# Performance work log

Measured on AMD Instinct MI355X. Metric: run time of the kernel, lower is better.

## Reference

```python
import jax, jax.numpy as jnp
import numpy as np

N = 100000
F_IN = 128
H = 64
E = 3200000


def setup_inputs() -> dict:
    key = jax.random.key(0)
    ks = jax.random.split(key, 10)
    x = jax.random.normal(ks[0], (N, F_IN), dtype=jnp.float32)
    edge_index = jax.random.randint(ks[1], (2, E), 0, N, dtype=jnp.int64)
    hidden_state = jax.random.normal(ks[2], (1, N, H), dtype=jnp.float32)
    # GCNConv params (glorot-ish scale)
    W_gcn = jax.random.normal(ks[3], (F_IN, H), dtype=jnp.float32) / np.sqrt(F_IN)
    b_gcn = jnp.zeros((H,), dtype=jnp.float32)
    # torch.nn.GRU params, layout [3H, in] with gate order (r, z, n)
    s = 1.0 / np.sqrt(H)
    W_ih = jax.random.uniform(ks[4], (3 * H, H), dtype=jnp.float32, minval=-s, maxval=s)
    W_hh = jax.random.uniform(ks[5], (3 * H, H), dtype=jnp.float32, minval=-s, maxval=s)
    b_ih = jax.random.uniform(ks[6], (3 * H,), dtype=jnp.float32, minval=-s, maxval=s)
    b_hh = jax.random.uniform(ks[7], (3 * H,), dtype=jnp.float32, minval=-s, maxval=s)
    return {"x": x, "edge_index": edge_index, "hidden_state": hidden_state,
            "W_gcn": W_gcn, "b_gcn": b_gcn,
            "W_ih": W_ih, "W_hh": W_hh, "b_ih": b_ih, "b_hh": b_hh}


def gcn_conv(x, edge_index, W, b):
    n = x.shape[0]
    # add self-loops (PyG GCNConv default)
    loops = jnp.arange(n, dtype=edge_index.dtype)
    row = jnp.concatenate([edge_index[0], loops])  # source
    col = jnp.concatenate([edge_index[1], loops])  # target
    # symmetric normalization: deg over targets with unit edge weights
    deg = jax.ops.segment_sum(jnp.ones_like(col, dtype=x.dtype), col, num_segments=n)
    dis = jnp.where(deg > 0, jax.lax.rsqrt(deg), 0.0)
    norm = dis[row] * dis[col]  # (E+N,)
    xt = x @ W  # (N, H) transform first, then aggregate
    msg = norm[:, None] * xt[row]  # (E+N, H)
    out = jax.ops.segment_sum(msg, col, num_segments=n)
    return out + b


def gru_step(x, h, W_ih, W_hh, b_ih, b_hh):
    # single-step torch GRU, gate order (r, z, n)
    gi = x @ W_ih.T + b_ih  # (N, 3H)
    gh = h @ W_hh.T + b_hh
    i_r, i_z, i_n = jnp.split(gi, 3, axis=-1)
    h_r, h_z, h_n = jnp.split(gh, 3, axis=-1)
    r = jax.nn.sigmoid(i_r + h_r)
    z = jax.nn.sigmoid(i_z + h_z)
    n = jnp.tanh(i_n + r * h_n)
    return (1.0 - z) * n + z * h


def reference(x, edge_index, hidden_state, W_gcn, b_gcn, W_ih, W_hh, b_ih, b_hh):
    g = jax.nn.relu(gcn_conv(x, edge_index, W_gcn, b_gcn))  # (N, H)
    h_new = gru_step(g, hidden_state[0], W_ih, W_hh, b_ih, b_hh)  # (N, H)
    return h_new, h_new[None]  # (out, new_hidden_state)
```

## Files before the change

### kernel.cpp

```cpp
#include <hip/hip_runtime.h>
#include <cmath>

constexpr int NN  = 100000;
constexpr int FIN = 128;
constexpr int HH  = 64;
constexpr int NE  = 3200000;
constexpr int NB  = (NN + 255) / 256;
constexpr int NFB  = NB;
constexpr int PCAP = 10240;

typedef __attribute__((ext_vector_type(8))) short short8;
typedef __attribute__((ext_vector_type(4))) float f32x4;

__device__ __forceinline__ ushort f2bf(float x) {
    unsigned u = __float_as_uint(x);
    u += 0x7FFF + ((u >> 16) & 1);
    return (ushort)(u >> 16);
}
__device__ __forceinline__ float bf2f(ushort h) {
    return __uint_as_float(((unsigned)h) << 16);
}
__device__ __forceinline__ unsigned pack2(float a, float b) {
    return (unsigned)f2bf(a) | ((unsigned)f2bf(b) << 16);
}

__global__ void __launch_bounds__(256) k_part(const int* __restrict__ ei,
                                              int* __restrict__ gcnt,
                                              int* __restrict__ pairs) {
    __shared__ int lcnt[NFB];
    __shared__ int lbase[NFB];
    int t = threadIdx.x;
    for (int i = t; i < NFB; i += 256) lcnt[i] = 0;
    __syncthreads();

    long long base = (long long)blockIdx.x * 8192;
    int4 r4[8], c4[8];
    int nv[8];
#pragma unroll
    for (int s = 0; s < 8; ++s) {
        long long e = base + s * 1024 + t * 4;
        if (e < NE) {
            r4[s] = ((const int4*)(ei))[e >> 2];
            c4[s] = ((const int4*)(ei + NE))[e >> 2];
            nv[s] = 1;
            atomicAdd(&lcnt[c4[s].x >> 8], 1);
            atomicAdd(&lcnt[c4[s].y >> 8], 1);
            atomicAdd(&lcnt[c4[s].z >> 8], 1);
            atomicAdd(&lcnt[c4[s].w >> 8], 1);
        } else {
            nv[s] = 0;
        }
    }
    __syncthreads();
    for (int i = t; i < NFB; i += 256) {
        int c = lcnt[i];
        lbase[i] = c ? atomicAdd(&gcnt[i], c) : 0;
        lcnt[i] = 0;
    }
    __syncthreads();
#pragma unroll
    for (int s = 0; s < 8; ++s) {
        if (!nv[s]) continue;
        int rr[4] = {r4[s].x, r4[s].y, r4[s].z, r4[s].w};
        int cc[4] = {c4[s].x, c4[s].y, c4[s].z, c4[s].w};
#pragma unroll
        for (int k = 0; k < 4; ++k) {
            int b   = cc[k] >> 8;
            int p   = atomicAdd(&lcnt[b], 1);
            int pos = lbase[b] + p;
            if (pos < PCAP) pairs[b * PCAP + pos] = (rr[k] << 8) | (cc[k] & 255);
        }
    }
}

__global__ void __launch_bounds__(256) k_csr(const int* __restrict__ pairs,
                                             const int* __restrict__ gcnt,
                                             int* __restrict__ deg,
                                             int* __restrict__ rowptr,
                                             float* __restrict__ dis,
                                             int* __restrict__ csr) {
    __shared__ int sg[256];
    __shared__ int ldeg[256];
    __shared__ int lrp[256];
    __shared__ int lcur[256];
    __shared__ int lcsr[PCAP];
    int f = blockIdx.x;
    int t = threadIdx.x;
    int partial = 0;
    if (t < f) partial += gcnt[t];
    if (t + 256 < f) partial += gcnt[t + 256];
    sg[t] = partial;
    ldeg[t] = 0;
    __syncthreads();
    for (int off = 128; off > 0; off >>= 1) {
        if (t < off) sg[t] += sg[t + off];
        __syncthreads();
    }
    int base = sg[0];
    int cnt  = min(gcnt[f], PCAP);
    int n0   = f * 256;
    const int* pb = pairs + f * PCAP;
    for (int i = t; i < cnt; i += 256) atomicAdd(&ldeg[pb[i] & 255], 1);
    __syncthreads();
    int v = ldeg[t];
    lrp[t] = v;
    __syncthreads();
    for (int off = 1; off < 256; off <<= 1) {
        int add = (t >= off) ? lrp[t - off] : 0;
        __syncthreads();
        lrp[t] += add;
        __syncthreads();
    }
    int excl = lrp[t] - v;
    if (n0 + t < NN) {
        deg[n0 + t]    = v;
        rowptr[n0 + t] = base + excl;
        dis[n0 + t]    = rsqrtf((float)(v + 1));
    }
    lcur[t] = excl;
    __syncthreads();
    for (int i = t; i < cnt; i += 256) {
        int e = pb[i];
        int p = atomicAdd(&lcur[e & 255], 1);
        lcsr[p] = e >> 8;
    }
    __syncthreads();
    for (int i = t; i < cnt; i += 256) csr[base + i] = lcsr[i];
}

__global__ void __launch_bounds__(256) k_xt(const float* __restrict__ x,
                                            const ushort* __restrict__ wgx,
                                            const float* __restrict__ dis,
                                            ushort* __restrict__ xtb) {
    __shared__ ushort Ahi[64 * 136];
    __shared__ ushort Alo[64 * 136];
    __shared__ float sdis[64];
    const ushort* GXhi = wgx;
    const ushort* GXlo = wgx + 64 * 128;
    int t  = threadIdx.x;
    int r0 = blockIdx.x * 64;
    if (t < 64) sdis[t] = (r0 + t < NN) ? dis[r0 + t] : 0.f;
    unsigned* Ahi32 = (unsigned*)Ahi;
    unsigned* Alo32 = (unsigned*)Alo;
#pragma unroll
    for (int s = 0; s < 8; ++s) {
        int idx = t + 256 * s;
        int nd  = idx >> 5;
        int kq  = idx & 31;
        bool ok = (r0 + nd) < NN;
        float4 v = ok ? ((const float4*)(x + (size_t)(r0 + nd) * FIN))[kq]
                      : make_float4(0.f, 0.f, 0.f, 0.f);
        int b2 = nd * 68 + kq * 2;
        float hx = bf2f(f2bf(v.x)), hy = bf2f(f2bf(v.y));
        float hz = bf2f(f2bf(v.z)), hw = bf2f(f2bf(v.w));
        Ahi32[b2]     = pack2(v.x, v.y);
        Ahi32[b2 + 1] = pack2(v.z, v.w);
        Alo32[b2]     = pack2(v.x - hx, v.y - hy);
        Alo32[b2 + 1] = pack2(v.z - hz, v.w - hw);
    }
    __syncthreads();

    int lane = t & 63, w = t >> 6, l15 = lane & 15;
    int kbase = (lane >> 4) * 8;
    int j = w * 16 + l15;
    f32x4 acc[4];
#pragma unroll
    for (int m = 0; m < 4; ++m) acc[m] = (f32x4){0.f, 0.f, 0.f, 0.f};
    short8 bh[4], bl[4];
#pragma unroll
    for (int ks = 0; ks < 4; ++ks) {
        bh[ks] = *(const short8*)(GXhi + j * 128 + ks * 32 + kbase);
        bl[ks] = *(const short8*)(GXlo + j * 128 + ks * 32 + kbase);
    }
#pragma unroll
    for (int mt = 0; mt < 4; ++mt) {
        int abase = (mt * 16 + l15) * 136 + kbase;
#pragma unroll
        for (int ks = 0; ks < 4; ++ks) {
            short8 ah = *(const short8*)&Ahi[abase + ks * 32];
            short8 al = *(const short8*)&Alo[abase + ks * 32];
            acc[mt] = __builtin_amdgcn_mfma_f32_16x16x32_bf16(ah, bh[ks], acc[mt], 0, 0, 0);
            acc[mt] = __builtin_amdgcn_mfma_f32_16x16x32_bf16(al, bh[ks], acc[mt], 0, 0, 0);
            acc[mt] = __builtin_amdgcn_mfma_f32_16x16x32_bf16(ah, bl[ks], acc[mt], 0, 0, 0);
        }
    }
    __syncthreads();
#pragma unroll
    for (int mt = 0; mt < 4; ++mt) {
#pragma unroll
        for (int reg = 0; reg < 4; ++reg) {
            int row = mt * 16 + (lane >> 4) * 4 + reg;
            Alo[row * 64 + j] = f2bf(sdis[row] * acc[mt][reg]);
        }
    }
    __syncthreads();
    const uint4* src = (const uint4*)Alo;
    uint4* dst = (uint4*)(xtb + (size_t)r0 * HH);
#pragma unroll
    for (int s = 0; s < 2; ++s) {
        int u   = t + 256 * s;
        int row = u >> 3;
        if (r0 + row < NN) dst[u] = src[u];
    }
}

__global__ void __launch_bounds__(256) k_gather(const int* __restrict__ csr,
                                                const int* __restrict__ rowptr,
                                                const int* __restrict__ deg,
                                                const float* __restrict__ dis,
                                                const ushort* __restrict__ xtb,
                                                const float* __restrict__ bg,
                                                float* __restrict__ g) {
    __shared__ int lid[4][64];
    int t    = threadIdx.x;
    int lane = t & 63;
    int w    = t >> 6;
    int n    = blockIdx.x * 4 + w;
    int r = lane >> 3;
    int q = lane & 7;
    float acc[8] = {0.f, 0.f, 0.f, 0.f, 0.f, 0.f, 0.f, 0.f};
    float dn  = dis[n];
    int start = rowptr[n];
    int cnt   = deg[n];
    for (int c0 = 0; c0 < cnt; c0 += 64) {
        int m = min(64, cnt - c0);
        if (lane < m) lid[w][lane] = csr[start + c0 + lane];
        int i = r;
        for (; i + 8 < m; i += 16) {
            int s0 = lid[w][i];
            int s1 = lid[w][i + 8];
            short8 v0 = ((const short8*)(xtb + (size_t)s0 * HH))[q];
            short8 v1 = ((const short8*)(xtb + (size_t)s1 * HH))[q];
#pragma unroll
            for (int j = 0; j < 8; ++j) acc[j] += bf2f((ushort)v0[j]);
#pragma unroll
            for (int j = 0; j < 8; ++j) acc[j] += bf2f((ushort)v1[j]);
        }
        if (i < m) {
            int s0 = lid[w][i];
            short8 v0 = ((const short8*)(xtb + (size_t)s0 * HH))[q];
#pragma unroll
            for (int j = 0; j < 8; ++j) acc[j] += bf2f((ushort)v0[j]);
        }
    }
#pragma unroll
    for (int j = 0; j < 8; ++j) {
        acc[j] += __shfl_xor(acc[j], 8, 64);
        acc[j] += __shfl_xor(acc[j], 16, 64);
        acc[j] += __shfl_xor(acc[j], 32, 64);
    }
    if (r == 0) {
        short8 xs = ((const short8*)(xtb + (size_t)n * HH))[q];
        float4 b0 = ((const float4*)bg)[q * 2];
        float4 b1 = ((const float4*)bg)[q * 2 + 1];
        float bb[8] = {b0.x, b0.y, b0.z, b0.w, b1.x, b1.y, b1.z, b1.w};
        float res[8];
#pragma unroll
        for (int j = 0; j < 8; ++j)
            res[j] = fmaxf(fmaf(dn, acc[j] + bf2f((ushort)xs[j]), bb[j]), 0.f);
        float4* go = (float4*)(g + (size_t)n * HH + q * 8);
        go[0] = make_float4(res[0], res[1], res[2], res[3]);
        go[1] = make_float4(res[4], res[5], res[6], res[7]);
    }
}

__global__ void k_wprep(const float* __restrict__ Wih, const float* __restrict__ Whh,
                        const float* __restrict__ Wg, ushort* __restrict__ bsp) {
    ushort* Bhi  = bsp;
    ushort* Blo  = bsp + 192 * 128;
    ushort* BShi = bsp + 2 * 192 * 128;
    ushort* BSlo = BShi + 64 * 64;
    ushort* GXhi = BSlo + 64 * 64;
    ushort* GXlo = GXhi + 64 * 128;
    int i = blockIdx.x * 256 + threadIdx.x;
    if (i < 192 * 128) {
        int j = i >> 7, k = i & 127;
        float wv = (k < 64) ? Wih[j * 64 + k] : Whh[j * 64 + (k - 64)];
        ushort hi = f2bf(wv);
        Bhi[i] = hi;
        Blo[i] = f2bf(wv - bf2f(hi));
    }
    if (i < 64 * 64) {
        int j = i >> 6, k = i & 63;
        float wv = Whh[(128 + j) * 64 + k];
        ushort hi = f2bf(wv);
        BShi[i] = hi;
        BSlo[i] = f2bf(wv - bf2f(hi));
    }
    if (i < 64 * 128) {
        int j = i >> 7, k = i & 127;
        float wv = Wg[k * HH + j];
        ushort hi = f2bf(wv);
        GXhi[i] = hi;
        GXlo[i] = f2bf(wv - bf2f(hi));
    }
}

__global__ void __launch_bounds__(256) k_gru(
    const float* __restrict__ gbuf, const float* __restrict__ hprev,
    const ushort* __restrict__ bsp,
    const float* __restrict__ bih, const float* __restrict__ bhh,
    float* __restrict__ out) {
    __shared__ ushort Ahi[32 * 136];
    __shared__ ushort Alo[32 * 136];
    const ushort* Bhi  = bsp;
    const ushort* Blo  = bsp + 192 * 128;
    const ushort* BShi = bsp + 2 * 192 * 128;
    const ushort* BSlo = BShi + 64 * 64;

    int t  = threadIdx.x;
    int n0 = blockIdx.x * 32;

    unsigned* Ahi32 = (unsigned*)Ahi;
    unsigned* Alo32 = (unsigned*)Alo;
#pragma unroll
    for (int s = 0; s < 2; ++s) {
        int idx = t + 256 * s;
        int nd  = idx >> 4;
        int kq  = idx & 15;
        bool ok = (n0 + nd) < NN;
        float4 vg = ok ? ((const float4*)(gbuf  + (size_t)(n0 + nd) * HH))[kq]
                       : make_float4(0.f, 0.f, 0.f, 0.f);
        float4 vh = ok ? ((const float4*)(hprev + (size_t)(n0 + nd) * HH))[kq]
                       : make_float4(0.f, 0.f, 0.f, 0.f);
        int bg2 = nd * 68 + kq * 2;
        int bh2 = bg2 + 32;
        float ghx = bf2f(f2bf(vg.x)), ghy = bf2f(f2bf(vg.y));
        float ghz = bf2f(f2bf(vg.z)), ghw = bf2f(f2bf(vg.w));
        float hhx = bf2f(f2bf(vh.x)), hhy = bf2f(f2bf(vh.y));
        float hhz = bf2f(f2bf(vh.z)), hhw = bf2f(f2bf(vh.w));
        Ahi32[bg2]     = pack2(vg.x, vg.y);
        Ahi32[bg2 + 1] = pack2(vg.z, vg.w);
        Alo32[bg2]     = pack2(vg.x - ghx, vg.y - ghy);
        Alo32[bg2 + 1] = pack2(vg.z - ghz, vg.w - ghw);
        Ahi32[bh2]     = pack2(vh.x, vh.y);
        Ahi32[bh2 + 1] = pack2(vh.z, vh.w);
        Alo32[bh2]     = pack2(vh.x - hhx, vh.y - hhy);
        Alo32[bh2 + 1] = pack2(vh.z - hhz, vh.w - hhw);
    }
    __syncthreads();

    int lane  = t & 63;
    int w     = t >> 6;
    int l15   = lane & 15;
    int kbase = (lane >> 4) * 8;

    f32x4 acc[4][2];
#pragma unroll
    for (int a = 0; a < 4; ++a)
#pragma unroll
        for (int m = 0; m < 2; ++m) acc[a][m] = (f32x4){0.f, 0.f, 0.f, 0.f};

#pragma unroll
    for (int g = 0; g < 3; ++g) {
        int brow = (w + 4 * g) * 16 + l15;
        short8 bh[4], bl[4];
#pragma unroll
        for (int ks = 0; ks < 4; ++ks) {
            bh[ks] = *(const short8*)(Bhi + brow * 128 + ks * 32 + kbase);
            bl[ks] = *(const short8*)(Blo + brow * 128 + ks * 32 + kbase);
        }
#pragma unroll
        for (int mt = 0; mt < 2; ++mt) {
            int abase = (mt * 16 + l15) * 136 + kbase;
#pragma unroll
            for (int ks = 0; ks < 4; ++ks) {
                short8 ah = *(const short8*)&Ahi[abase + ks * 32];
                short8 al = *(const short8*)&Alo[abase + ks * 32];
                acc[g][mt] = __builtin_amdgcn_mfma_f32_16x16x32_bf16(ah, bh[ks], acc[g][mt], 0, 0, 0);
                acc[g][mt] = __builtin_amdgcn_mfma_f32_16x16x32_bf16(al, bh[ks], acc[g][mt], 0, 0, 0);
                acc[g][mt] = __builtin_amdgcn_mfma_f32_16x16x32_bf16(ah, bl[ks], acc[g][mt], 0, 0, 0);
            }
        }
    }
    {
        int brow = w * 16 + l15;
        short8 bh[2], bl[2];
#pragma unroll
        for (int ks = 0; ks < 2; ++ks) {
            bh[ks] = *(const short8*)(BShi + brow * 64 + ks * 32 + kbase);
            bl[ks] = *(const short8*)(BSlo + brow * 64 + ks * 32 + kbase);
        }
#pragma unroll
        for (int mt = 0; mt < 2; ++mt) {
            int abase = (mt * 16 + l15) * 136 + 64 + kbase;
#pragma unroll
            for (int ks = 0; ks < 2; ++ks) {
                short8 ah = *(const short8*)&Ahi[abase + ks * 32];
                short8 al = *(const short8*)&Alo[abase + ks * 32];
                acc[3][mt] = __builtin_amdgcn_mfma_f32_16x16x32_bf16(ah, bh[ks], acc[3][mt], 0, 0, 0);
                acc[3][mt] = __builtin_amdgcn_mfma_f32_16x16x32_bf16(al, bh[ks], acc[3][mt], 0, 0, 0);
                acc[3][mt] = __builtin_amdgcn_mfma_f32_16x16x32_bf16(ah, bl[ks], acc[3][mt], 0, 0, 0);
            }
        }
    }

    int j = 16 * w + l15;
    float br  = bih[j] + bhh[j];
    float bz  = bih[HH + j] + bhh[HH + j];
    float bin = bih[2 * HH + j];
    float bhn = bhh[2 * HH + j];
#pragma unroll
    for (int mt = 0; mt < 2; ++mt) {
#pragma unroll
        for (int reg = 0; reg < 4; ++reg) {
            int row  = mt * 16 + (lane >> 4) * 4 + reg;
            int node = n0 + row;
            if (node < NN) {
                float S1 = acc[0][mt][reg];
                float S2 = acc[1][mt][reg];
                float S3 = acc[2][mt][reg];
                float Hn = acc[3][mt][reg];
                float r  = __builtin_amdgcn_rcpf(1.f + __expf(-(S1 + br)));
                float z  = __builtin_amdgcn_rcpf(1.f + __expf(-(S2 + bz)));
                float na = (S3 - Hn + bin) + r * (Hn + bhn);
                float e2 = __expf(2.f * na);
                float nv = fmaf(-2.f, __builtin_amdgcn_rcpf(1.f + e2), 1.f);
                int lidx = row * 136 + 64 + j;
                float h  = bf2f(Ahi[lidx]) + bf2f(Alo[lidx]);
                float o  = (1.f - z) * nv + z * h;
                out[(size_t)node * HH + j] = o;
                out[(size_t)NN * HH + (size_t)node * HH + j] = o;
            }
        }
    }
}

extern "C" void kernel_launch(void* const* d_in, const int* in_sizes, int n_in,
                              void* d_out, int out_size, void* d_ws, size_t ws_size,
                              hipStream_t stream) {
    const float* x   = (const float*)d_in[0];
    const int*   ei  = (const int*)d_in[1];
    const float* hs  = (const float*)d_in[2];
    const float* Wg  = (const float*)d_in[3];
    const float* bg  = (const float*)d_in[4];
    const float* Wih = (const float*)d_in[5];
    const float* Whh = (const float*)d_in[6];
    const float* bih = (const float*)d_in[7];
    const float* bhh = (const float*)d_in[8];
    float* out = (float*)d_out;

    char* ws = (char*)d_ws;
    int*    pairs  = (int*)   (ws);
    ushort* xtb    = (ushort*)(ws);
    float*  gbuf   = (float*) (ws + 16400000);
    int*    csr    = (int*)   (ws + 42000000);
    int*    deg    = (int*)   (ws + 54800000);
    int*    rowptr = (int*)   (ws + 55200000);
    float*  dis    = (float*) (ws + 55600000);
    ushort* wsplit = (ushort*)(ws + 56000000);
    int*    gcnt   = (int*)   (ws + 56200000);

    hipMemsetAsync(gcnt, 0, NFB * sizeof(int), stream);

    hipLaunchKernelGGL(k_wprep, dim3(96), dim3(256), 0, stream, Wih, Whh, Wg, wsplit);
    hipLaunchKernelGGL(k_part,  dim3((NE + 8191) / 8192), dim3(256), 0, stream, ei, gcnt, pairs);
    hipLaunchKernelGGL(k_csr,   dim3(NFB), dim3(256), 0, stream,
                       pairs, gcnt, deg, rowptr, dis, csr);
    hipLaunchKernelGGL(k_xt,    dim3((NN + 63) / 64), dim3(256), 0, stream,
                       x, wsplit + 2 * 192 * 128 + 2 * 64 * 64, dis, xtb);
    hipLaunchKernelGGL(k_gather, dim3(NN / 4), dim3(256), 0, stream,
                       csr, rowptr, deg, dis, xtb, bg, gbuf);
    hipLaunchKernelGGL(k_gru,   dim3((NN + 31) / 32), dim3(256), 0, stream,
                       gbuf, hs, wsplit, bih, bhh, out);
}
```

Baseline: 321.3 us.

## Fuse GCN neighbor gather into GRU kernel via shared-memory staging

Merges the gather/aggregate kernel and the GRU MFMA kernel into one 512-thread kernel that handles 64 nodes per block. Each wave aggregates 8 nodes and writes the ReLU output, split into bf16 hi/lo parts, straight into shared memory, so the fp32 intermediate buffer no longer goes through global memory and one launch is removed. In exchange, each wave now walks 8 nodes serially and the block is larger with more shared memory, which may lower occupancy and reduce latency hiding for the irregular gather.

```diff
diff --git a/kernel.cpp b/kernel.cpp
--- a/kernel.cpp
+++ b/kernel.cpp
@@ -204,66 +204,6 @@
     }
 }
 
-__global__ void __launch_bounds__(256) k_gather(const int* __restrict__ csr,
-                                                const int* __restrict__ rowptr,
-                                                const int* __restrict__ deg,
-                                                const float* __restrict__ dis,
-                                                const ushort* __restrict__ xtb,
-                                                const float* __restrict__ bg,
-                                                float* __restrict__ g) {
-    __shared__ int lid[4][64];
-    int t    = threadIdx.x;
-    int lane = t & 63;
-    int w    = t >> 6;
-    int n    = blockIdx.x * 4 + w;
-    int r = lane >> 3;
-    int q = lane & 7;
-    float acc[8] = {0.f, 0.f, 0.f, 0.f, 0.f, 0.f, 0.f, 0.f};
-    float dn  = dis[n];
-    int start = rowptr[n];
-    int cnt   = deg[n];
-    for (int c0 = 0; c0 < cnt; c0 += 64) {
-        int m = min(64, cnt - c0);
-        if (lane < m) lid[w][lane] = csr[start + c0 + lane];
-        int i = r;
-        for (; i + 8 < m; i += 16) {
-            int s0 = lid[w][i];
-            int s1 = lid[w][i + 8];
-            short8 v0 = ((const short8*)(xtb + (size_t)s0 * HH))[q];
-            short8 v1 = ((const short8*)(xtb + (size_t)s1 * HH))[q];
-#pragma unroll
-            for (int j = 0; j < 8; ++j) acc[j] += bf2f((ushort)v0[j]);
-#pragma unroll
-            for (int j = 0; j < 8; ++j) acc[j] += bf2f((ushort)v1[j]);
-        }
-        if (i < m) {
-            int s0 = lid[w][i];
-            short8 v0 = ((const short8*)(xtb + (size_t)s0 * HH))[q];
-#pragma unroll
-            for (int j = 0; j < 8; ++j) acc[j] += bf2f((ushort)v0[j]);
-        }
-    }
-#pragma unroll
-    for (int j = 0; j < 8; ++j) {
-        acc[j] += __shfl_xor(acc[j], 8, 64);
-        acc[j] += __shfl_xor(acc[j], 16, 64);
-        acc[j] += __shfl_xor(acc[j], 32, 64);
-    }
-    if (r == 0) {
-        short8 xs = ((const short8*)(xtb + (size_t)n * HH))[q];
-        float4 b0 = ((const float4*)bg)[q * 2];
-        float4 b1 = ((const float4*)bg)[q * 2 + 1];
-        float bb[8] = {b0.x, b0.y, b0.z, b0.w, b1.x, b1.y, b1.z, b1.w};
-        float res[8];
-#pragma unroll
-        for (int j = 0; j < 8; ++j)
-            res[j] = fmaxf(fmaf(dn, acc[j] + bf2f((ushort)xs[j]), bb[j]), 0.f);
-        float4* go = (float4*)(g + (size_t)n * HH + q * 8);
-        go[0] = make_float4(res[0], res[1], res[2], res[3]);
-        go[1] = make_float4(res[4], res[5], res[6], res[7]);
-    }
-}
-
 __global__ void k_wprep(const float* __restrict__ Wih, const float* __restrict__ Whh,
                         const float* __restrict__ Wg, ushort* __restrict__ bsp) {
     ushort* Bhi  = bsp;
@@ -296,54 +236,118 @@
     }
 }
 
-__global__ void __launch_bounds__(256) k_gru(
-    const float* __restrict__ gbuf, const float* __restrict__ hprev,
-    const ushort* __restrict__ bsp,
+__global__ void __launch_bounds__(512) k_gg(
+    const int* __restrict__ csr, const int* __restrict__ rowptr,
+    const int* __restrict__ deg, const float* __restrict__ dis,
+    const ushort* __restrict__ xtb, const float* __restrict__ bg,
+    const float* __restrict__ hprev, const ushort* __restrict__ bsp,
     const float* __restrict__ bih, const float* __restrict__ bhh,
     float* __restrict__ out) {
-    __shared__ ushort Ahi[32 * 136];
-    __shared__ ushort Alo[32 * 136];
+    __shared__ ushort Ahi[64 * 136];
+    __shared__ ushort Alo[64 * 136];
+    __shared__ int lid[8][64];
     const ushort* Bhi  = bsp;
     const ushort* Blo  = bsp + 192 * 128;
     const ushort* BShi = bsp + 2 * 192 * 128;
     const ushort* BSlo = BShi + 64 * 64;
 
-    int t  = threadIdx.x;
-    int n0 = blockIdx.x * 32;
+    int t    = threadIdx.x;
+    int w    = t >> 6;
+    int lane = t & 63;
+    int n0   = blockIdx.x * 64;
 
     unsigned* Ahi32 = (unsigned*)Ahi;
     unsigned* Alo32 = (unsigned*)Alo;
+
 #pragma unroll
     for (int s = 0; s < 2; ++s) {
-        int idx = t + 256 * s;
+        int idx = t + 512 * s;
         int nd  = idx >> 4;
         int kq  = idx & 15;
         bool ok = (n0 + nd) < NN;
-        float4 vg = ok ? ((const float4*)(gbuf  + (size_t)(n0 + nd) * HH))[kq]
-                       : make_float4(0.f, 0.f, 0.f, 0.f);
         float4 vh = ok ? ((const float4*)(hprev + (size_t)(n0 + nd) * HH))[kq]
                        : make_float4(0.f, 0.f, 0.f, 0.f);
-        int bg2 = nd * 68 + kq * 2;
-        int bh2 = bg2 + 32;
-        float ghx = bf2f(f2bf(vg.x)), ghy = bf2f(f2bf(vg.y));
-        float ghz = bf2f(f2bf(vg.z)), ghw = bf2f(f2bf(vg.w));
-        float hhx = bf2f(f2bf(vh.x)), hhy = bf2f(f2bf(vh.y));
-        float hhz = bf2f(f2bf(vh.z)), hhw = bf2f(f2bf(vh.w));
-        Ahi32[bg2]     = pack2(vg.x, vg.y);
-        Ahi32[bg2 + 1] = pack2(vg.z, vg.w);
-        Alo32[bg2]     = pack2(vg.x - ghx, vg.y - ghy);
-        Alo32[bg2 + 1] = pack2(vg.z - ghz, vg.w - ghw);
-        Ahi32[bh2]     = pack2(vh.x, vh.y);
-        Ahi32[bh2 + 1] = pack2(vh.z, vh.w);
-        Alo32[bh2]     = pack2(vh.x - hhx, vh.y - hhy);
-        Alo32[bh2 + 1] = pack2(vh.z - hhz, vh.w - hhw);
-    }
-    __syncthreads();
-
-    int lane  = t & 63;
-    int w     = t >> 6;
+        int b2 = nd * 68 + 32 + kq * 2;
+        float hx = bf2f(f2bf(vh.x)), hy = bf2f(f2bf(vh.y));
+        float hz = bf2f(f2bf(vh.z)), hw = bf2f(f2bf(vh.w));
+        Ahi32[b2]     = pack2(vh.x, vh.y);
+        Ahi32[b2 + 1] = pack2(vh.z, vh.w);
+        Alo32[b2]     = pack2(vh.x - hx, vh.y - hy);
+        Alo32[b2 + 1] = pack2(vh.z - hz, vh.w - hw);
+    }
+
+    int r = lane >> 3;
+    int q = lane & 7;
+#pragma unroll 1
+    for (int i = 0; i < 8; ++i) {
+        int nd = w * 8 + i;
+        int n  = n0 + nd;
+        if (n >= NN) break;
+        float accv[8] = {0.f, 0.f, 0.f, 0.f, 0.f, 0.f, 0.f, 0.f};
+        int start = rowptr[n];
+        int cnt   = deg[n];
+        for (int c0 = 0; c0 < cnt; c0 += 64) {
+            int m = min(64, cnt - c0);
+            if (lane < m) lid[w][lane] = csr[start + c0 + lane];
+            int ii = r;
+            for (; ii + 8 < m; ii += 16) {
+                int s0 = lid[w][ii];
+                int s1 = lid[w][ii + 8];
+                short8 v0 = ((const short8*)(xtb + (size_t)s0 * HH))[q];
+                short8 v1 = ((const short8*)(xtb + (size_t)s1 * HH))[q];
+#pragma unroll
+                for (int j = 0; j < 8; ++j) accv[j] += bf2f((ushort)v0[j]);
+#pragma unroll
+                for (int j = 0; j < 8; ++j) accv[j] += bf2f((ushort)v1[j]);
+            }
+            if (ii < m) {
+                int s0 = lid[w][ii];
+                short8 v0 = ((const short8*)(xtb + (size_t)s0 * HH))[q];
+#pragma unroll
+                for (int j = 0; j < 8; ++j) accv[j] += bf2f((ushort)v0[j]);
+            }
+        }
+#pragma unroll
+        for (int j = 0; j < 8; ++j) {
+            accv[j] += __shfl_xor(accv[j], 8, 64);
+            accv[j] += __shfl_xor(accv[j], 16, 64);
+            accv[j] += __shfl_xor(accv[j], 32, 64);
+        }
+        if (r == 0) {
+            float dn = dis[n];
+            short8 xs = ((const short8*)(xtb + (size_t)n * HH))[q];
+            float4 b0 = ((const float4*)bg)[q * 2];
+            float4 b1 = ((const float4*)bg)[q * 2 + 1];
+            float bb[8] = {b0.x, b0.y, b0.z, b0.w, b1.x, b1.y, b1.z, b1.w};
+            float res[8];
+            ushort hi[8];
+            float lo[8];
+#pragma unroll
+            for (int j = 0; j < 8; ++j) {
+                res[j] = fmaxf(fmaf(dn, accv[j] + bf2f((ushort)xs[j]), bb[j]), 0.f);
+                hi[j]  = f2bf(res[j]);
+                lo[j]  = res[j] - bf2f(hi[j]);
+            }
+            int b32 = nd * 68 + q * 4;
+            uint4 uh, ul;
+            uh.x = (unsigned)hi[0] | ((unsigned)hi[1] << 16);
+            uh.y = (unsigned)hi[2] | ((unsigned)hi[3] << 16);
+            uh.z = (unsigned)hi[4] | ((unsigned)hi[5] << 16);
+            uh.w = (unsigned)hi[6] | ((unsigned)hi[7] << 16);
+            ul.x = pack2(lo[0], lo[1]);
+            ul.y = pack2(lo[2], lo[3]);
+            ul.z = pack2(lo[4], lo[5]);
+            ul.w = pack2(lo[6], lo[7]);
+            *(uint4*)&Ahi32[b32] = uh;
+            *(uint4*)&Alo32[b32] = ul;
+        }
+    }
+    __syncthreads();
+
     int l15   = lane & 15;
     int kbase = (lane >> 4) * 8;
+    int mh    = w >> 2;
+    int wj    = w & 3;
 
     f32x4 acc[4][2];
 #pragma unroll
@@ -353,7 +357,7 @@
 
 #pragma unroll
     for (int g = 0; g < 3; ++g) {
-        int brow = (w + 4 * g) * 16 + l15;
+        int brow = (wj + 4 * g) * 16 + l15;
         short8 bh[4], bl[4];
 #pragma unroll
         for (int ks = 0; ks < 4; ++ks) {
@@ -362,7 +366,7 @@
         }
 #pragma unroll
         for (int mt = 0; mt < 2; ++mt) {
-            int abase = (mt * 16 + l15) * 136 + kbase;
+            int abase = (mh * 32 + mt * 16 + l15) * 136 + kbase;
 #pragma unroll
             for (int ks = 0; ks < 4; ++ks) {
                 short8 ah = *(const short8*)&Ahi[abase + ks * 32];
@@ -374,7 +378,7 @@
         }
     }
     {
-        int brow = w * 16 + l15;
+        int brow = wj * 16 + l15;
         short8 bh[2], bl[2];
 #pragma unroll
         for (int ks = 0; ks < 2; ++ks) {
@@ -383,7 +387,7 @@
         }
 #pragma unroll
         for (int mt = 0; mt < 2; ++mt) {
-            int abase = (mt * 16 + l15) * 136 + 64 + kbase;
+            int abase = (mh * 32 + mt * 16 + l15) * 136 + 64 + kbase;
 #pragma unroll
             for (int ks = 0; ks < 2; ++ks) {
                 short8 ah = *(const short8*)&Ahi[abase + ks * 32];
@@ -395,7 +399,7 @@
         }
     }
 
-    int j = 16 * w + l15;
+    int j = wj * 16 + l15;
     float br  = bih[j] + bhh[j];
     float bz  = bih[HH + j] + bhh[HH + j];
     float bin = bih[2 * HH + j];
@@ -404,16 +408,16 @@
     for (int mt = 0; mt < 2; ++mt) {
 #pragma unroll
         for (int reg = 0; reg < 4; ++reg) {
-            int row  = mt * 16 + (lane >> 4) * 4 + reg;
+            int row  = mh * 32 + mt * 16 + (lane >> 4) * 4 + reg;
             int node = n0 + row;
             if (node < NN) {
                 float S1 = acc[0][mt][reg];
                 float S2 = acc[1][mt][reg];
                 float S3 = acc[2][mt][reg];
                 float Hn = acc[3][mt][reg];
-                float r  = __builtin_amdgcn_rcpf(1.f + __expf(-(S1 + br)));
+                float rr = __builtin_amdgcn_rcpf(1.f + __expf(-(S1 + br)));
                 float z  = __builtin_amdgcn_rcpf(1.f + __expf(-(S2 + bz)));
-                float na = (S3 - Hn + bin) + r * (Hn + bhn);
+                float na = (S3 - Hn + bin) + rr * (Hn + bhn);
                 float e2 = __expf(2.f * na);
                 float nv = fmaf(-2.f, __builtin_amdgcn_rcpf(1.f + e2), 1.f);
                 int lidx = row * 136 + 64 + j;
@@ -443,7 +447,6 @@
     char* ws = (char*)d_ws;
     int*    pairs  = (int*)   (ws);
     ushort* xtb    = (ushort*)(ws);
-    float*  gbuf   = (float*) (ws + 16400000);
     int*    csr    = (int*)   (ws + 42000000);
     int*    deg    = (int*)   (ws + 54800000);
     int*    rowptr = (int*)   (ws + 55200000);
@@ -459,8 +462,6 @@
                        pairs, gcnt, deg, rowptr, dis, csr);
     hipLaunchKernelGGL(k_xt,    dim3((NN + 63) / 64), dim3(256), 0, stream,
                        x, wsplit + 2 * 192 * 128 + 2 * 64 * 64, dis, xtb);
-    hipLaunchKernelGGL(k_gather, dim3(NN / 4), dim3(256), 0, stream,
-                       csr, rowptr, deg, dis, xtb, bg, gbuf);
-    hipLaunchKernelGGL(k_gru,   dim3((NN + 31) / 32), dim3(256), 0, stream,
-                       gbuf, hs, wsplit, bih, bhh, out);
-}
+    hipLaunchKernelGGL(k_gg,    dim3((NN + 63) / 64), dim3(512), 0, stream,
+                       csr, rowptr, deg, dis, xtb, bg, hs, wsplit, bih, bhh, out);
+}
```

New measurement: 355.4 us. 10.6% more time.
